# Kernel tuning notes

Hardware: AMD Instinct MI355X
Metric: run time of the kernel (lower is better)

Reference implementation:

```python
import jax, jax.numpy as jnp
import numpy as np

PS = 32    # base patch size
SUB = 16   # subdivided patch size produced by sigmoid_round for up-weighted patches


def _sigmoid_round_np(x):
    # mirrors torch: round(32*sigmoid(x-24) + 16*(1-sigmoid(x-24)))
    s = 1.0 / (1.0 + np.exp(-(x - 24.0)))
    return np.round(32.0 * s + 16.0 * (1.0 - s)).astype(np.int64)


def _build_importance(P):
    # deterministic importance weights: even patches slightly above the mean
    # (-> adaptive size 16, subdivided), odd patches below (-> size 32, kept).
    avg = 1.0 / P
    a = avg * (2.0 ** (1.0 / 12.0)) * 1.001
    b = 2.0 * avg - a
    iw = np.empty(P, np.float64)
    iw[0::2] = a
    iw[1::2] = b
    return iw


def _build_token_index(P, G):
    # Reproduces the torch module's per-patch structural decision at trace time
    # (numpy on deterministic constants -> static shapes, jit-safe).
    iw = _build_importance(P)
    avg = iw.mean()
    sizes = _sigmoid_round_np(PS * (avg ** 12) / (iw ** 12))
    tok = []
    for i in range(P):
        r, c = i // G, i % G
        if 7 < sizes[i] < PS:  # subdivided into (PS/SUB)^2 = 4 sub-patches, row-major
            for dr in range(PS // SUB):
                for dc in range(PS // SUB):
                    tok.append(G * G + (2 * r + dr) * (2 * G) + (2 * c + dc))
        else:                   # full 32x32 patch token
            tok.append(r * G + c)
    return np.asarray(tok, np.int32)


def setup_inputs() -> dict:
    key = jax.random.key(0)
    k1, k2, k3 = jax.random.split(key, 3)
    B, C, H, E = 32, 3, 512, 768
    x = jax.random.normal(k1, (B, C, H, H), jnp.float32)
    patch_weight = jax.random.normal(k2, (E, C, PS, PS), jnp.float32) * 0.02
    patch_bias = jax.random.normal(k3, (E,), jnp.float32) * 0.02
    P = (H // PS) ** 2
    importance_w = jnp.asarray(_build_importance(P), jnp.float32)
    return {"x": x, "importance_w": importance_w, "patch_weight": patch_weight,
            "patch_bias": patch_bias, "num_patches": P}


def reference(x, importance_w, patch_weight, patch_bias, num_patches):
    B, C, H, _ = x.shape
    E = patch_weight.shape[0]
    G = H // PS            # 32x32 patch grid side
    kd = PS // SUB         # kernel divisor = 2
    tok_idx = _build_token_index(num_patches, G)  # static gather structure

    # full-size patches: stride-PS conv on each 32x32 tile == one GEMM
    # x tiles: (b, c, r, i, q, j) with row = r*PS+i, col = q*PS+j
    full = jnp.einsum('bcriqj,ecij->brqe',
                      x.reshape(B, C, G, PS, G, PS), patch_weight) + patch_bias

    # averaged 16x16 kernel: view(E,C,kd,kd,SUB,SUB).mean(dim=2).mean(dim=2)
    w_sub = patch_weight.reshape(E, C, kd, kd, SUB, SUB).mean(axis=(2, 3))
    sub = jnp.einsum('bcriqj,ecij->brqe',
                     x.reshape(B, C, kd * G, SUB, kd * G, SUB), w_sub) + patch_bias

    # token pool: [full 32-tiles (G*G), then all 16-tiles ((2G)^2)]; gather in
    # original patch order with subdivided patches expanded in place.
    pool = jnp.concatenate([full.reshape(B, G * G, E),
                            sub.reshape(B, (kd * G) ** 2, E)], axis=1)
    return pool[:, tok_idx, :]
```

## Files before the change

### kernel.cpp

```cpp
#include <hip/hip_runtime.h>
#include <stdint.h>


typedef __attribute__((ext_vector_type(8))) short bf16x8;
typedef __attribute__((ext_vector_type(4))) float f32x4;

__device__ __forceinline__ unsigned short f2bf(float f) {
  union { float f; unsigned u; } v; v.f = f;
  return (unsigned short)((v.u + 0x7fffu + ((v.u >> 16) & 1u)) >> 16);
}
__device__ __forceinline__ float bf2f(unsigned short h) {
  union { unsigned u; float f; } v; v.u = ((unsigned)h) << 16; return v.f;
}

__global__ __launch_bounds__(256) void prep_gather(
    const float* __restrict__ x, const float* __restrict__ pw,
    unsigned short* __restrict__ Wf, unsigned short* __restrict__ Ws,
    unsigned short* __restrict__ Af, unsigned short* __restrict__ Asub) {
  int bid = blockIdx.x, t = threadIdx.x;
  if (bid < 2304) {
    int g = bid * 256 + t;
    float4 v = ((const float4*)pw)[g];
    ((ushort4*)Wf)[g] = make_ushort4(f2bf(v.x), f2bf(v.y), f2bf(v.z), f2bf(v.w));
  } else if (bid < 2880) {
    int g = (bid - 2304) * 256 + t;
    int e = g / 192;
    int rem = g - e * 192;
    int cc = rem >> 6, r2 = rem & 63, s = r2 >> 2, t4 = r2 & 3;
    const float* base = pw + ((size_t)((e * 3 + cc) * 32 + (s >> 1)) * 32
                              + 16 * (s & 1) + 4 * t4);
    float4 q0 = *(const float4*)(base);
    float4 q1 = *(const float4*)(base + 8 * 32);
    float4 q2 = *(const float4*)(base + 16 * 32);
    float4 q3 = *(const float4*)(base + 24 * 32);
    ((ushort4*)Ws)[g] = make_ushort4(
        f2bf(0.25f * (q0.x + q1.x + q2.x + q3.x)),
        f2bf(0.25f * (q0.y + q1.y + q2.y + q3.y)),
        f2bf(0.25f * (q0.z + q1.z + q2.z + q3.z)),
        f2bf(0.25f * (q0.w + q1.w + q2.w + q3.w)));
  } else if (bid < 15168) {
    int g = (bid - 2880) * 256 + t;
    int m = g / 768, q = g - m * 768;
    int b = m >> 7, p = m & 127;
    int i = 2 * p + 1;
    int r = i >> 4, cpat = i & 15;
    int cc = q >> 8, rem = q & 255, ii = rem >> 3, jj4 = rem & 7;
    const float4* src = (const float4*)(x + ((size_t)((b * 3 + cc) * 512 + (r * 32 + ii)) * 512
                                             + cpat * 32 + jj4 * 4));
    float4 v = *src;
    ((ushort4*)Af)[g] = make_ushort4(f2bf(v.x), f2bf(v.y), f2bf(v.z), f2bf(v.w));
  } else {
    int g = (bid - 15168) * 256 + t;
    int m = g / 192, q = g - m * 192;
    int b = m >> 9, tt = m & 511;
    int p = tt >> 2, s = tt & 3, dr = s >> 1, dc = s & 1;
    int i = 2 * p;
    int r = i >> 4, cpat = i & 15;
    int cc = q >> 6, rem = q & 63, ii = rem >> 2, jj4 = rem & 3;
    int srow = r * 32 + dr * 16 + ii;
    int scol = cpat * 32 + dc * 16 + jj4 * 4;
    const float4* src = (const float4*)(x + ((size_t)((b * 3 + cc) * 512 + srow) * 512 + scol));
    float4 v = *src;
    ((ushort4*)Asub)[g] = make_ushort4(f2bf(v.x), f2bf(v.y), f2bf(v.z), f2bf(v.w));
  }
}

__global__ __launch_bounds__(256) void gemm_kernel(
    const unsigned short* __restrict__ Af, const unsigned short* __restrict__ Asub,
    const unsigned short* __restrict__ Wf, const unsigned short* __restrict__ Ws,
    const float* __restrict__ bias, unsigned short* __restrict__ Pf,
    float* __restrict__ out) {
  __shared__ unsigned short Asm[128 * 64];
  __shared__ unsigned short Bsm[128 * 64];

  int bid = (blockIdx.x & 7) * 192 + (blockIdx.x >> 3);

  const unsigned short* Abase;
  const unsigned short* Bbase;
  int rsA, bm, bn, kofs, which, kc = 0;
  if (bid < 768) {
    which = 0;
    int grp = bid / 6; bn = bid - grp * 6;
    bm = grp >> 2; kc = grp & 3;
    rsA = 3072; kofs = kc * 768;
    Abase = Af + (size_t)bm * 128 * 3072;
    Bbase = Wf;
  } else {
    which = 1;
    int id = bid - 768;
    bm = id / 6; bn = id - bm * 6;
    rsA = 768; kofs = 0;
    Abase = Asub + (size_t)bm * 128 * 768;
    Bbase = Ws;
  }
  const unsigned short* Brow = Bbase + (size_t)bn * 128 * rsA;

  int t = threadIdx.x;
  int lane = t & 63;
  int wv = t >> 6, wr = wv >> 1, wc = wv & 1;
  int lr = lane & 15, lk = lane >> 4;

  f32x4 acc[4][4];
#pragma unroll
  for (int mm = 0; mm < 4; ++mm)
#pragma unroll
    for (int nn = 0; nn < 4; ++nn) acc[mm][nn] = (f32x4){0.f, 0.f, 0.f, 0.f};

  const unsigned short* a_src = Abase + (size_t)(t >> 3) * rsA + (t & 7) * 8 + kofs;
  const unsigned short* b_src = Brow + (size_t)(t >> 3) * rsA + (t & 7) * 8 + kofs;
  unsigned short* as_dst = &Asm[t * 8];
  unsigned short* bs_dst = &Bsm[t * 8];

  for (int k0 = 0; k0 < 768; k0 += 64) {
#pragma unroll
    for (int is = 0; is < 4; ++is) {
      __builtin_amdgcn_global_load_lds(
          (const __attribute__((address_space(1))) void*)(a_src + (size_t)is * 32 * rsA + k0),
          (__attribute__((address_space(3))) void*)(as_dst + is * 2048), 16, 0, 0);
      __builtin_amdgcn_global_load_lds(
          (const __attribute__((address_space(1))) void*)(b_src + (size_t)is * 32 * rsA + k0),
          (__attribute__((address_space(3))) void*)(bs_dst + is * 2048), 16, 0, 0);
    }
    __syncthreads();
#pragma unroll
    for (int kk = 0; kk < 64; kk += 32) {
      bf16x8 af[4], bf[4];
#pragma unroll
      for (int mm = 0; mm < 4; ++mm)
        af[mm] = *(const bf16x8*)&Asm[(wr * 64 + mm * 16 + lr) * 64 + kk + lk * 8];
#pragma unroll
      for (int nn = 0; nn < 4; ++nn)
        bf[nn] = *(const bf16x8*)&Bsm[(wc * 64 + nn * 16 + lr) * 64 + kk + lk * 8];
#pragma unroll
      for (int mm = 0; mm < 4; ++mm)
#pragma unroll
        for (int nn = 0; nn < 4; ++nn)
          acc[mm][nn] = __builtin_amdgcn_mfma_f32_16x16x32_bf16(af[mm], bf[nn], acc[mm][nn], 0, 0, 0);
    }
    __syncthreads();
  }

#pragma unroll
  for (int mm = 0; mm < 4; ++mm) {
    int trow = wr * 64 + mm * 16 + lk * 4;
#pragma unroll
    for (int reg = 0; reg < 4; ++reg) {
      int grow = bm * 128 + trow + reg;
      if (which == 0) {
        unsigned short* pdst = Pf + ((size_t)(kc * 4096 + grow)) * 768;
#pragma unroll
        for (int nn = 0; nn < 4; ++nn) {
          int gcol = bn * 128 + wc * 64 + nn * 16 + lr;
          pdst[gcol] = f2bf(acc[mm][nn][reg]);
        }
      } else {
        int b = grow >> 9, tt2 = grow & 511, p = tt2 >> 2, s = tt2 & 3;
        size_t obase = (size_t)(b * 640 + 5 * p + s) * 768;
#pragma unroll
        for (int nn = 0; nn < 4; ++nn) {
          int gcol = bn * 128 + wc * 64 + nn * 16 + lr;
          out[obase + gcol] = acc[mm][nn][reg] + bias[gcol];
        }
      }
    }
  }
}

__global__ __launch_bounds__(256) void reduce_full(
    const unsigned short* __restrict__ Pf, const float* __restrict__ bias,
    float* __restrict__ out) {
  int q = blockIdx.x * 256 + threadIdx.x;
  int m = q / 192, c4 = q - m * 192;
  float4 sacc = ((const float4*)bias)[c4];
#pragma unroll
  for (int kc = 0; kc < 4; ++kc) {
    ushort4 u = ((const ushort4*)(Pf + ((size_t)(kc * 4096 + m)) * 768))[c4];
    sacc.x += bf2f(u.x); sacc.y += bf2f(u.y);
    sacc.z += bf2f(u.z); sacc.w += bf2f(u.w);
  }
  int b = m >> 7, p = m & 127;
  size_t obase = (size_t)(b * 640 + 5 * p + 4) * 768;
  ((float4*)(out + obase))[c4] = sacc;
}

extern "C" void kernel_launch(void* const* d_in, const int* in_sizes, int n_in,
                              void* d_out, int out_size, void* d_ws, size_t ws_size,
                              hipStream_t stream) {
  const float* x  = (const float*)d_in[0];
  const float* pw = (const float*)d_in[2];
  const float* pb = (const float*)d_in[3];
  float* out = (float*)d_out;

  unsigned short* Af   = (unsigned short*)d_ws;
  unsigned short* Asub = Af + 12582912;
  unsigned short* Wf   = Asub + 12582912;
  unsigned short* Ws   = Wf + 2359296;
  unsigned short* Pf   = Ws + 589824;

  prep_gather<<<27456, 256, 0, stream>>>(x, pw, Wf, Ws, Af, Asub);
  gemm_kernel<<<1536, 256, 0, stream>>>(Af, Asub, Wf, Ws, pb, Pf, out);
  reduce_full<<<3072, 256, 0, stream>>>(Pf, pb, out);
}
```

Before: 255.2 us.

## Fuse input patch gather and bf16 conversion into the GEMM A-tile load

Drops the separate gather pass that converted x patches to bf16 in workspace. The GEMM now reads fp32 x directly with per-row patch address math, converts to bf16 in registers and stores the result to LDS, while B keeps using async global-to-LDS loads. This removes a full write and re-read of about 50 MB of bf16 activations. In exchange the A loads become synchronous register loads with no async LDS path, and the x reads are strided.

```diff
diff --git a/kernel.cpp b/kernel.cpp
--- a/kernel.cpp
+++ b/kernel.cpp
@@ -3,6 +3,7 @@
 
 
 typedef __attribute__((ext_vector_type(8))) short bf16x8;
+typedef __attribute__((ext_vector_type(8))) unsigned short ushort8;
 typedef __attribute__((ext_vector_type(4))) float f32x4;
 
 __device__ __forceinline__ unsigned short f2bf(float f) {
@@ -13,16 +14,15 @@
   union { unsigned u; float f; } v; v.u = ((unsigned)h) << 16; return v.f;
 }
 
-__global__ __launch_bounds__(256) void prep_gather(
-    const float* __restrict__ x, const float* __restrict__ pw,
-    unsigned short* __restrict__ Wf, unsigned short* __restrict__ Ws,
-    unsigned short* __restrict__ Af, unsigned short* __restrict__ Asub) {
+__global__ __launch_bounds__(256) void prep_w(const float* __restrict__ pw,
+                                              unsigned short* __restrict__ Wf,
+                                              unsigned short* __restrict__ Ws) {
   int bid = blockIdx.x, t = threadIdx.x;
   if (bid < 2304) {
     int g = bid * 256 + t;
     float4 v = ((const float4*)pw)[g];
     ((ushort4*)Wf)[g] = make_ushort4(f2bf(v.x), f2bf(v.y), f2bf(v.z), f2bf(v.w));
-  } else if (bid < 2880) {
+  } else {
     int g = (bid - 2304) * 256 + t;
     int e = g / 192;
     int rem = g - e * 192;
@@ -38,35 +38,11 @@
         f2bf(0.25f * (q0.y + q1.y + q2.y + q3.y)),
         f2bf(0.25f * (q0.z + q1.z + q2.z + q3.z)),
         f2bf(0.25f * (q0.w + q1.w + q2.w + q3.w)));
-  } else if (bid < 15168) {
-    int g = (bid - 2880) * 256 + t;
-    int m = g / 768, q = g - m * 768;
-    int b = m >> 7, p = m & 127;
-    int i = 2 * p + 1;
-    int r = i >> 4, cpat = i & 15;
-    int cc = q >> 8, rem = q & 255, ii = rem >> 3, jj4 = rem & 7;
-    const float4* src = (const float4*)(x + ((size_t)((b * 3 + cc) * 512 + (r * 32 + ii)) * 512
-                                             + cpat * 32 + jj4 * 4));
-    float4 v = *src;
-    ((ushort4*)Af)[g] = make_ushort4(f2bf(v.x), f2bf(v.y), f2bf(v.z), f2bf(v.w));
-  } else {
-    int g = (bid - 15168) * 256 + t;
-    int m = g / 192, q = g - m * 192;
-    int b = m >> 9, tt = m & 511;
-    int p = tt >> 2, s = tt & 3, dr = s >> 1, dc = s & 1;
-    int i = 2 * p;
-    int r = i >> 4, cpat = i & 15;
-    int cc = q >> 6, rem = q & 63, ii = rem >> 2, jj4 = rem & 3;
-    int srow = r * 32 + dr * 16 + ii;
-    int scol = cpat * 32 + dc * 16 + jj4 * 4;
-    const float4* src = (const float4*)(x + ((size_t)((b * 3 + cc) * 512 + srow) * 512 + scol));
-    float4 v = *src;
-    ((ushort4*)Asub)[g] = make_ushort4(f2bf(v.x), f2bf(v.y), f2bf(v.z), f2bf(v.w));
-  }
-}
-
-__global__ __launch_bounds__(256) void gemm_kernel(
-    const unsigned short* __restrict__ Af, const unsigned short* __restrict__ Asub,
+  }
+}
+
+__global__ __launch_bounds__(256) void gemm_fused(
+    const float* __restrict__ x,
     const unsigned short* __restrict__ Wf, const unsigned short* __restrict__ Ws,
     const float* __restrict__ bias, unsigned short* __restrict__ Pf,
     float* __restrict__ out) {
@@ -75,51 +51,79 @@
 
   int bid = (blockIdx.x & 7) * 192 + (blockIdx.x >> 3);
 
-  const unsigned short* Abase;
   const unsigned short* Bbase;
-  int rsA, bm, bn, kofs, which, kc = 0;
+  int rsB, bm, bn, kofs, which, kc = 0;
+  int ccsh, iish, iimask, jjmask;
   if (bid < 768) {
     which = 0;
     int grp = bid / 6; bn = bid - grp * 6;
     bm = grp >> 2; kc = grp & 3;
-    rsA = 3072; kofs = kc * 768;
-    Abase = Af + (size_t)bm * 128 * 3072;
+    rsB = 3072; kofs = kc * 768;
     Bbase = Wf;
+    ccsh = 10; iish = 5; iimask = 31; jjmask = 31;
   } else {
     which = 1;
     int id = bid - 768;
     bm = id / 6; bn = id - bm * 6;
-    rsA = 768; kofs = 0;
-    Abase = Asub + (size_t)bm * 128 * 768;
+    rsB = 768; kofs = 0;
     Bbase = Ws;
-  }
-  const unsigned short* Brow = Bbase + (size_t)bn * 128 * rsA;
+    ccsh = 8; iish = 4; iimask = 15; jjmask = 15;
+  }
 
   int t = threadIdx.x;
   int lane = t & 63;
   int wv = t >> 6, wr = wv >> 1, wc = wv & 1;
   int lr = lane & 15, lk = lane >> 4;
 
-  f32x4 acc[4][4];
-#pragma unroll
-  for (int mm = 0; mm < 4; ++mm)
-#pragma unroll
-    for (int nn = 0; nn < 4; ++nn) acc[mm][nn] = (f32x4){0.f, 0.f, 0.f, 0.f};
-
-  const unsigned short* a_src = Abase + (size_t)(t >> 3) * rsA + (t & 7) * 8 + kofs;
-  const unsigned short* b_src = Brow + (size_t)(t >> 3) * rsA + (t & 7) * 8 + kofs;
+  int kbase = kofs + (t & 7) * 8;
+  int abase[4];
+#pragma unroll
+  for (int is = 0; is < 4; ++is) {
+    int m = bm * 128 + (t >> 3) + is * 32;
+    int b, r, cp, extra;
+    if (which == 0) {
+      b = m >> 7; int p = m & 127; int i = 2 * p + 1;
+      r = i >> 4; cp = i & 15; extra = 0;
+    } else {
+      b = m >> 9; int q = m & 511; int p = q >> 2, s = q & 3;
+      int dr = s >> 1, dc = s & 1; int i = 2 * p;
+      r = i >> 4; cp = i & 15; extra = dr * 8192 + dc * 16;
+    }
+    abase[is] = b * 786432 + r * 16384 + cp * 32 + extra;
+  }
+  const unsigned short* b_src = Bbase + (size_t)(bn * 128 + (t >> 3)) * rsB
+                                + (t & 7) * 8 + kofs;
   unsigned short* as_dst = &Asm[t * 8];
   unsigned short* bs_dst = &Bsm[t * 8];
 
+  f32x4 acc[4][4];
+#pragma unroll
+  for (int mm = 0; mm < 4; ++mm)
+#pragma unroll
+    for (int nn = 0; nn < 4; ++nn) acc[mm][nn] = (f32x4){0.f, 0.f, 0.f, 0.f};
+
   for (int k0 = 0; k0 < 768; k0 += 64) {
 #pragma unroll
+    for (int is = 0; is < 4; ++is)
+      __builtin_amdgcn_global_load_lds(
+          (const __attribute__((address_space(1))) void*)(b_src + (size_t)is * 32 * rsB + k0),
+          (__attribute__((address_space(3))) void*)(bs_dst + is * 2048), 16, 0, 0);
+    float4 va[4][2];
+    int k = kbase + k0;
+    int koff = (k >> ccsh) * 262144 + ((k >> iish) & iimask) * 512 + (k & jjmask);
+#pragma unroll
     for (int is = 0; is < 4; ++is) {
-      __builtin_amdgcn_global_load_lds(
-          (const __attribute__((address_space(1))) void*)(a_src + (size_t)is * 32 * rsA + k0),
-          (__attribute__((address_space(3))) void*)(as_dst + is * 2048), 16, 0, 0);
-      __builtin_amdgcn_global_load_lds(
-          (const __attribute__((address_space(1))) void*)(b_src + (size_t)is * 32 * rsA + k0),
-          (__attribute__((address_space(3))) void*)(bs_dst + is * 2048), 16, 0, 0);
+      const float4* s4 = (const float4*)(x + abase[is] + koff);
+      va[is][0] = s4[0]; va[is][1] = s4[1];
+    }
+#pragma unroll
+    for (int is = 0; is < 4; ++is) {
+      ushort8 v;
+      v[0] = f2bf(va[is][0].x); v[1] = f2bf(va[is][0].y);
+      v[2] = f2bf(va[is][0].z); v[3] = f2bf(va[is][0].w);
+      v[4] = f2bf(va[is][1].x); v[5] = f2bf(va[is][1].y);
+      v[6] = f2bf(va[is][1].z); v[7] = f2bf(va[is][1].w);
+      *(ushort8*)(as_dst + is * 2048) = v;
     }
     __syncthreads();
 #pragma unroll
@@ -191,13 +195,11 @@
   const float* pb = (const float*)d_in[3];
   float* out = (float*)d_out;
 
-  unsigned short* Af   = (unsigned short*)d_ws;
-  unsigned short* Asub = Af + 12582912;
-  unsigned short* Wf   = Asub + 12582912;
-  unsigned short* Ws   = Wf + 2359296;
-  unsigned short* Pf   = Ws + 589824;
-
-  prep_gather<<<27456, 256, 0, stream>>>(x, pw, Wf, Ws, Af, Asub);
-  gemm_kernel<<<1536, 256, 0, stream>>>(Af, Asub, Wf, Ws, pb, Pf, out);
+  unsigned short* Wf = (unsigned short*)d_ws;
+  unsigned short* Ws = Wf + 2359296;
+  unsigned short* Pf = Ws + 589824;
+
+  prep_w<<<2880, 256, 0, stream>>>(pw, Wf, Ws);
+  gemm_fused<<<1536, 256, 0, stream>>>(x, Wf, Ws, pb, Pf, out);
   reduce_full<<<3072, 256, 0, stream>>>(Pf, pb, out);
 }
```

Result: faster. 244.6 us (-4.1%).
